# Kernel optimization log

Hardware: AMD Instinct MI355X
Metric: run time of the kernel (lower is better)

The kernel has to match this reference:

```python
import jax, jax.numpy as jnp
import numpy as np

NTYPES = 2
MAXNEI = 128      # maxNeighborNum
M2 = 16
NPER = 256        # atoms per type
B = 4
EMB = [25, 50, 100]
FIT_IN = M2 * EMB[-1]  # 1600
FH = 240


def setup_inputs() -> dict:
    key = jax.random.key(0)
    ks = jax.random.split(key, 16)
    s = 0.1
    inp = {
        "Ri": jax.random.normal(ks[0], (B, NTYPES * NPER, NTYPES * MAXNEI, 4), jnp.float32),
        "emb_W0": jax.random.normal(ks[1], (4, 1, EMB[0]), jnp.float32) * s,
        "emb_b0": jax.random.normal(ks[2], (4, EMB[0]), jnp.float32) * s,
        "emb_W1": jax.random.normal(ks[3], (4, EMB[0], EMB[1]), jnp.float32) * s,
        "emb_b1": jax.random.normal(ks[4], (4, EMB[1]), jnp.float32) * s,
        "emb_W2": jax.random.normal(ks[5], (4, EMB[1], EMB[2]), jnp.float32) * s,
        "emb_b2": jax.random.normal(ks[6], (4, EMB[2]), jnp.float32) * s,
        "fit_W0": jax.random.normal(ks[7], (2, FIT_IN, FH), jnp.float32) * 0.02,
        "fit_b0": jax.random.normal(ks[8], (2, FH), jnp.float32) * s,
        "fit_W1": jax.random.normal(ks[9], (2, FH, FH), jnp.float32) * 0.05,
        "fit_b1": jax.random.normal(ks[10], (2, FH), jnp.float32) * s,
        "fit_W2": jax.random.normal(ks[11], (2, FH, FH), jnp.float32) * 0.05,
        "fit_b2": jax.random.normal(ks[12], (2, FH), jnp.float32) * s,
        "fit_W3": jax.random.normal(ks[13], (2, FH, 1), jnp.float32) * 0.05,
        "fit_b3": jax.random.normal(ks[14], (2, 1), jnp.float32),
    }
    return inp


def _emb(s, W0, b0, W1, b1, W2, b2):
    # DeepMD-style embedding MLP with doubling resnet skips (1->25->50->100)
    h0 = jnp.tanh(s @ W0 + b0)
    h1 = jnp.tanh(h0 @ W1 + b1) + jnp.concatenate([h0, h0], axis=-1)
    h2 = jnp.tanh(h1 @ W2 + b2) + jnp.concatenate([h1, h1], axis=-1)
    return h2


def _fit(d, W0, b0, W1, b1, W2, b2, W3, b3):
    h = jnp.tanh(d @ W0 + b0)
    h = jnp.tanh(h @ W1 + b1) + h   # resnet skip (equal dims)
    h = jnp.tanh(h @ W2 + b2) + h
    return h @ W3 + b3              # [B, N, 1]


def reference(Ri, emb_W0, emb_b0, emb_W1, emb_b1, emb_W2, emb_b2,
              fit_W0, fit_b0, fit_W1, fit_b1, fit_W2, fit_b2, fit_W3, fit_b3):
    type_nums = NTYPES
    Ei_blocks = []
    for i in range(NTYPES):                      # center-atom type
        Ri_i = Ri[:, i * NPER:(i + 1) * NPER]    # [B, NPER, NTYPES*M, 4]
        xyz = None
        for j in range(NTYPES):                  # neighbor type
            blk = Ri_i[:, :, j * MAXNEI:(j + 1) * MAXNEI, :]  # [B,N,M,4]
            S = blk[..., 0:1]                                  # [B,N,M,1]
            e = i * NTYPES + j
            G = _emb(S, emb_W0[e], emb_b0[e], emb_W1[e], emb_b1[e],
                     emb_W2[e], emb_b2[e])                     # [B,N,M,100]
            tmp = jnp.einsum('bnmc,bnmg->bncg', blk, G)        # [B,N,4,100]
            xyz = tmp if xyz is None else xyz + tmp
        xyz = xyz / (MAXNEI * type_nums)
        xyz_b = xyz[..., :M2]                                  # [B,N,4,16]
        DR = jnp.einsum('bncg,bnch->bngh', xyz, xyz_b)         # [B,N,100,16]
        DR = DR.reshape(B, NPER, FIT_IN)
        Ei_i = _fit(DR, fit_W0[i], fit_b0[i], fit_W1[i], fit_b1[i],
                    fit_W2[i], fit_b2[i], fit_W3[i], fit_b3[i])  # [B,N,1]
        Ei_blocks.append(Ei_i)
    Ei = jnp.concatenate(Ei_blocks, axis=1)     # [B, natoms_sum, 1]
    return Ei[..., 0]                            # per-atom energies [B, natoms_sum]
```

## Files before the change

kernel.cpp:

```cpp
#include <hip/hip_runtime.h>
#include <hip/hip_bf16.h>

#define FH 240
#define FIT_IN 1600
#define NK 2048
#define TLO -16.0f
#define TINVH 64.0f

typedef _Float16 h8 __attribute__((ext_vector_type(8)));
typedef float f4v __attribute__((ext_vector_type(4)));

__device__ __forceinline__ float fast_tanh(float x) {
    float e2 = __builtin_amdgcn_exp2f(x * 2.8853900817779268f);
    return 1.0f - 2.0f * __builtin_amdgcn_rcpf(e2 + 1.0f);
}

#define FMA_ROW(r, s) \
    acc[r][0] += (s) * b0.x; acc[r][1] += (s) * b0.y; \
    acc[r][2] += (s) * b0.z; acc[r][3] += (s) * b0.w; \
    acc[r][4] += (s) * b1.x; acc[r][5] += (s) * b1.y; \
    acc[r][6] += (s) * b1.z; acc[r][7] += (s) * b1.w;

#define TOFF_W0   0
#define TOFF_B0   28
#define TOFF_B1   56
#define TOFF_B2   108
#define TOFF_W1   208
#define TOFF_W2   1508
#define TOFF_H0T  6708
#define TOFF_H1T  10008
#define TSMEM     16608

__global__ __launch_bounds__(256) void k_prep(
    const float* __restrict__ eW0, const float* __restrict__ eB0,
    const float* __restrict__ eW1, const float* __restrict__ eB1,
    const float* __restrict__ eW2, const float* __restrict__ eB2,
    float* __restrict__ T,
    const float* __restrict__ fW0, const float* __restrict__ fW1,
    const float* __restrict__ fW2,
    _Float16* __restrict__ W0T, _Float16* __restrict__ W1T,
    _Float16* __restrict__ W2T)
{
    __shared__ float sm[TSMEM];
    const int t = threadIdx.x;

    if (blockIdx.x >= 64) {
        const int bid0 = blockIdx.x - 64;
        const int total = 768000 + 115200 + 115200;
        for (int idx = bid0 * 256 + t; idx < total; idx += 448 * 256) {
            if (idx < 768000) {
                const int tp = idx / 384000, r = idx - tp * 384000;
                const int n = r / 1600, k = r - n * 1600;
                W0T[idx] = (_Float16)fW0[tp * 384000 + k * 240 + n];
            } else if (idx < 883200) {
                const int j = idx - 768000;
                const int tp = j / 57600, r = j - tp * 57600;
                const int n = r / 240, k = r - n * 240;
                W1T[j] = (_Float16)fW1[tp * 57600 + k * 240 + n];
            } else {
                const int j = idx - 883200;
                const int tp = j / 57600, r = j - tp * 57600;
                const int n = r / 240, k = r - n * 240;
                W2T[j] = (_Float16)fW2[tp * 57600 + k * 240 + n];
            }
        }
        return;
    }

    const int w    = t >> 6;
    const int lane = t & 63;
    const int mi   = lane & 7;
    const int gi   = lane >> 3;
    const int mrow = w * 32 + mi * 4;

    const int e  = blockIdx.x >> 4;
    const int k0 = (blockIdx.x & 15) * 128;

    for (int idx = t; idx < 1250; idx += 256) {
        int k = idx / 50, g = idx - k * 50;
        sm[TOFF_W1 + k * 52 + g] = eW1[e * 1250 + idx];
    }
    for (int idx = t; idx < 5000; idx += 256) {
        int k = idx / 100, r = idx - k * 100;
        int half = r / 50, g = r - half * 50;
        sm[TOFF_W2 + k * 104 + half * 52 + g] = eW2[e * 5000 + idx];
    }
    if (t < 25)       { sm[TOFF_W0 + t] = eW0[e * 25 + t]; sm[TOFF_B0 + t] = eB0[e * 25 + t]; }
    else if (t < 75)  { sm[TOFF_B1 + (t - 25)] = eB1[e * 50 + (t - 25)]; }
    else if (t < 175) { sm[TOFF_B2 + (t - 75)] = eB2[e * 100 + (t - 75)]; }
    __syncthreads();

    if (t < 128) {
        const float S = TLO + (float)(k0 + t) * (1.0f / TINVH);
        #pragma unroll
        for (int k = 0; k < 25; ++k)
            sm[TOFF_H0T + k * 132 + t] = fast_tanh(S * sm[TOFF_W0 + k] + sm[TOFF_B0 + k]);
    }
    __syncthreads();

    {
        float acc[4][8];
        #pragma unroll
        for (int r = 0; r < 4; ++r)
            #pragma unroll
            for (int c = 0; c < 8; ++c) acc[r][c] = 0.f;

        #pragma unroll 5
        for (int k = 0; k < 25; ++k) {
            const float4 av = *(const float4*)&sm[TOFF_H0T + k * 132 + mrow];
            const float4 b0 = *(const float4*)&sm[TOFF_W1 + k * 52 + gi * 8];
            const float4 b1 = *(const float4*)&sm[TOFF_W1 + k * 52 + gi * 8 + 4];
            FMA_ROW(0, av.x) FMA_ROW(1, av.y) FMA_ROW(2, av.z) FMA_ROW(3, av.w)
        }
        #pragma unroll
        for (int c = 0; c < 8; ++c) {
            const int g = gi * 8 + c;
            if (g < 50) {
                const int gm = (g < 25) ? g : g - 25;
                const float4 h0r = *(const float4*)&sm[TOFF_H0T + gm * 132 + mrow];
                const float bias = sm[TOFF_B1 + g];
                float4 o;
                o.x = fast_tanh(acc[0][c] + bias) + h0r.x;
                o.y = fast_tanh(acc[1][c] + bias) + h0r.y;
                o.z = fast_tanh(acc[2][c] + bias) + h0r.z;
                o.w = fast_tanh(acc[3][c] + bias) + h0r.w;
                *(float4*)&sm[TOFF_H1T + g * 132 + mrow] = o;
            }
        }
    }
    __syncthreads();

    for (int half = 0; half < 2; ++half) {
        float acc[4][8];
        #pragma unroll
        for (int r = 0; r < 4; ++r)
            #pragma unroll
            for (int c = 0; c < 8; ++c) acc[r][c] = 0.f;

        #pragma unroll 5
        for (int k = 0; k < 50; ++k) {
            const float4 av = *(const float4*)&sm[TOFF_H1T + k * 132 + mrow];
            const float4 b0 = *(const float4*)&sm[TOFF_W2 + k * 104 + half * 52 + gi * 8];
            const float4 b1 = *(const float4*)&sm[TOFF_W2 + k * 104 + half * 52 + gi * 8 + 4];
            FMA_ROW(0, av.x) FMA_ROW(1, av.y) FMA_ROW(2, av.z) FMA_ROW(3, av.w)
        }
        #pragma unroll
        for (int c = 0; c < 8; ++c) {
            const int g = gi * 8 + c;
            if (g < 50) {
                const float4 h1r = *(const float4*)&sm[TOFF_H1T + g * 132 + mrow];
                const float bias = sm[TOFF_B2 + half * 50 + g];
                float* out = T + ((size_t)e * NK + k0 + mrow) * 100 + half * 50 + g;
                out[0]   = fast_tanh(acc[0][c] + bias) + h1r.x;
                out[100] = fast_tanh(acc[1][c] + bias) + h1r.y;
                out[200] = fast_tanh(acc[2][c] + bias) + h1r.z;
                out[300] = fast_tanh(acc[3][c] + bias) + h1r.w;
            }
        }
    }
}

__global__ __launch_bounds__(256) void k_xyz(
    const float* __restrict__ Ri, const float* __restrict__ T,
    _Float16* __restrict__ DRh)
{
    __shared__ float4 sR[256];
    __shared__ float  sF[256];
    __shared__ int    sI[256];
    __shared__ float  sXYZ[400];

    const int t   = threadIdx.x;
    const int blk = blockIdx.x;
    const int b   = blk >> 9;
    const int i   = (blk >> 8) & 1;
    const int n   = blk & 255;

    for (int idx = t; idx < 400; idx += 256) sXYZ[idx] = 0.f;

    {
        const int jj = t >> 7, m = t & 127;
        const size_t row = ((size_t)(b * 512 + i * 256 + n)) * 256 + jj * 128 + m;
        const float4 r = *(const float4*)(Ri + row * 4);
        sR[t] = r;
        float u = (r.x - TLO) * TINVH;
        int ii = (int)u;
        ii = (ii < 0) ? 0 : ((ii > NK - 2) ? NK - 2 : ii);
        sI[t] = ii;
        sF[t] = u - (float)ii;
    }
    __syncthreads();

    const int jj = t >> 7;
    const int g  = t & 127;
    if (g < 100) {
        const float* Te = T + ((size_t)(i * 2 + jj)) * NK * 100 + g;
        float a0 = 0.f, a1 = 0.f, a2 = 0.f, a3 = 0.f;
        #pragma unroll 4
        for (int m = 0; m < 128; ++m) {
            const int s = jj * 128 + m;
            const float4 R = sR[s];
            const float  f = sF[s];
            const float* p = Te + (size_t)sI[s] * 100;
            const float v0 = p[0], v1 = p[100];
            const float G = v0 + f * (v1 - v0);
            a0 += R.x * G; a1 += R.y * G; a2 += R.z * G; a3 += R.w * G;
        }
        atomicAdd(&sXYZ[g],       a0);
        atomicAdd(&sXYZ[100 + g], a1);
        atomicAdd(&sXYZ[200 + g], a2);
        atomicAdd(&sXYZ[300 + g], a3);
    }
    __syncthreads();

    const float inv = 1.0f / 65536.0f;
    _Float16* dr = DRh + (((size_t)i * 4 + b) * 256 + n) * FIT_IN;
    for (int q = t; q < 400; q += 256) {
        const int gg = q >> 2, h0 = (q & 3) * 4;
        ushort4 pk;
        _Float16* ph = (_Float16*)&pk;
        #pragma unroll
        for (int r = 0; r < 4; ++r) {
            const int h = h0 + r;
            const float v = (sXYZ[gg] * sXYZ[h] + sXYZ[100 + gg] * sXYZ[100 + h]
                           + sXYZ[200 + gg] * sXYZ[200 + h] + sXYZ[300 + gg] * sXYZ[300 + h]) * inv;
            ph[r] = (_Float16)v;
        }
        *(ushort4*)(dr + gg * 16 + h0) = pk;
    }
}

__global__ __launch_bounds__(512) void k_fit(
    const _Float16* __restrict__ DRh,
    const _Float16* __restrict__ W0T, const _Float16* __restrict__ W1T,
    const _Float16* __restrict__ W2T,
    const float* __restrict__ fb0, const float* __restrict__ fb1,
    const float* __restrict__ fb2, const float* __restrict__ fW3,
    const float* __restrict__ fb3, float* __restrict__ out)
{
    __shared__ _Float16 sA[16 * 264];
    __shared__ float    hRes[2][8 * 240];

    const int t    = threadIdx.x;
    const int w    = t >> 6;
    const int lane = t & 63;
    const int ln   = lane & 15;
    const int quad = lane >> 4;
    const int r0   = blockIdx.x * 8;
    const int tp   = r0 >> 10;
    const int nf0  = w * 2;
    const int nfr  = (w < 7) ? 2 : 1;

    for (int q = t; q < 16 * 264; q += 512) sA[q] = (_Float16)0.f;

    f4v acc[2];
    acc[0] = (f4v)0.f; acc[1] = (f4v)0.f;
    {
        const _Float16* Arow = DRh + (size_t)(r0 + (ln & 7)) * FIT_IN;
        const _Float16* W0b  = W0T + (size_t)tp * 240 * FIT_IN;
        const _Float16* Bp0  = W0b + (size_t)(nf0 * 16 + ln) * FIT_IN;
        const _Float16* Bp1  = W0b + (size_t)(((nfr > 1) ? nf0 + 1 : nf0) * 16 + ln) * FIT_IN;
        const int kq = quad * 8;

        h8 a_c  = *(const h8*)(Arow + kq);
        h8 b0_c = *(const h8*)(Bp0 + kq);
        h8 b1_c = *(const h8*)(Bp1 + kq);
        h8 a_n  = *(const h8*)(Arow + 32 + kq);
        h8 b0_n = *(const h8*)(Bp0 + 32 + kq);
        h8 b1_n = *(const h8*)(Bp1 + 32 + kq);

        #pragma unroll 2
        for (int s = 0; s < 50; ++s) {
            h8 a_f, b0_f, b1_f;
            if (s + 2 < 50) {
                const int k2 = (s + 2) * 32 + kq;
                a_f  = *(const h8*)(Arow + k2);
                b0_f = *(const h8*)(Bp0 + k2);
                b1_f = *(const h8*)(Bp1 + k2);
            }
            acc[0] = __builtin_amdgcn_mfma_f32_16x16x32_f16(a_c, b0_c, acc[0], 0, 0, 0);
            acc[1] = __builtin_amdgcn_mfma_f32_16x16x32_f16(a_c, b1_c, acc[1], 0, 0, 0);
            a_c = a_n;  b0_c = b0_n;  b1_c = b1_n;
            a_n = a_f;  b0_n = b0_f;  b1_n = b1_f;
        }
    }
    {
        const float* B0 = fb0 + tp * FH;
        #pragma unroll
        for (int nf = 0; nf < 2; ++nf) {
            if (nf < nfr && quad < 2) {
                const int col = (nf0 + nf) * 16 + ln;
                const float bias = B0[col];
                #pragma unroll
                for (int r = 0; r < 4; ++r) {
                    const int m = quad * 4 + r;
                    const float v = fast_tanh(acc[nf][r] + bias);
                    hRes[0][m * 240 + col] = v;
                    sA[m * 264 + col] = (_Float16)v;
                }
            }
        }
    }
    __syncthreads();

    for (int layer = 0; layer < 2; ++layer) {
        const _Float16* Wt = (layer == 0 ? W1T : W2T) + (size_t)tp * FH * FH;
        const float* Bias  = (layer == 0 ? fb1 : fb2) + tp * FH;
        const float* res   = hRes[layer];
        float* outb        = hRes[layer ^ 1];

        const _Float16* Bq0 = Wt + (size_t)(nf0 * 16 + ln) * FH;
        const _Float16* Bq1 = Wt + (size_t)(((nfr > 1) ? nf0 + 1 : nf0) * 16 + ln) * FH;
        const int kq = quad * 8;

        f4v a2[2];
        a2[0] = (f4v)0.f; a2[1] = (f4v)0.f;

        h8 b0_c = *(const h8*)(Bq0 + kq);
        h8 b1_c = *(const h8*)(Bq1 + kq);
        #pragma unroll
        for (int s = 0; s < 8; ++s) {
            h8 b0_n, b1_n;
            if (s + 1 < 8) {
                const int k1 = (s + 1) * 32 + kq;
                b0_n = *(const h8*)(Bq0 + k1);
                b1_n = *(const h8*)(Bq1 + k1);
            }
            const h8 afr = *(const h8*)&sA[ln * 264 + s * 32 + kq];
            a2[0] = __builtin_amdgcn_mfma_f32_16x16x32_f16(afr, b0_c, a2[0], 0, 0, 0);
            a2[1] = __builtin_amdgcn_mfma_f32_16x16x32_f16(afr, b1_c, a2[1], 0, 0, 0);
            b0_c = b0_n;  b1_c = b1_n;
        }
        __syncthreads();
        #pragma unroll
        for (int nf = 0; nf < 2; ++nf) {
            if (nf < nfr && quad < 2) {
                const int col = (nf0 + nf) * 16 + ln;
                const float bias = Bias[col];
                #pragma unroll
                for (int r = 0; r < 4; ++r) {
                    const int m = quad * 4 + r;
                    const float v = fast_tanh(a2[nf][r] + bias) + res[m * 240 + col];
                    outb[m * 240 + col] = v;
                    if (layer == 0) sA[m * 264 + col] = (_Float16)v;
                }
            }
        }
        __syncthreads();
    }

    {
        const float* h2 = hRes[0];
        const float* wv = fW3 + tp * FH;
        const int m = w;
        float s = 0.f;
        #pragma unroll
        for (int k = lane; k < FH; k += 64) s += h2[m * 240 + k] * wv[k];
        #pragma unroll
        for (int off = 32; off > 0; off >>= 1) s += __shfl_down(s, off);
        if (lane == 0) {
            const int gr = r0 + m;
            const int rem = gr & 1023;
            const int b = rem >> 8, n = rem & 255;
            out[b * 512 + tp * 256 + n] = s + fb3[tp];
        }
    }
}

extern "C" void kernel_launch(void* const* d_in, const int* in_sizes, int n_in,
                              void* d_out, int out_size, void* d_ws, size_t ws_size,
                              hipStream_t stream)
{
    const float* Ri  = (const float*)d_in[0];
    const float* eW0 = (const float*)d_in[1];
    const float* eB0 = (const float*)d_in[2];
    const float* eW1 = (const float*)d_in[3];
    const float* eB1 = (const float*)d_in[4];
    const float* eW2 = (const float*)d_in[5];
    const float* eB2 = (const float*)d_in[6];
    const float* fW0 = (const float*)d_in[7];
    const float* fb0 = (const float*)d_in[8];
    const float* fW1 = (const float*)d_in[9];
    const float* fb1 = (const float*)d_in[10];
    const float* fW2 = (const float*)d_in[11];
    const float* fb2 = (const float*)d_in[12];
    const float* fW3 = (const float*)d_in[13];
    const float* fb3 = (const float*)d_in[14];

    char* p = (char*)d_ws;
    float* T   = (float*)p;                 p += (size_t)4 * NK * 100 * 4;
    _Float16* DRh = (_Float16*)p;           p += (size_t)2048 * FIT_IN * 2;
    _Float16* W0T = (_Float16*)p;           p += (size_t)768000 * 2;
    _Float16* W1T = (_Float16*)p;           p += (size_t)115200 * 2;
    _Float16* W2T = (_Float16*)p;           p += (size_t)115200 * 2;

    k_prep<<<dim3(512), dim3(256), 0, stream>>>(eW0, eB0, eW1, eB1, eW2, eB2, T,
                                                fW0, fW1, fW2, W0T, W1T, W2T);
    k_xyz<<<dim3(2048), dim3(256), 0, stream>>>(Ri, T, DRh);
    k_fit<<<dim3(256), dim3(512), 0, stream>>>(DRh, W0T, W1T, W2T,
                                               fb0, fb1, fb2, fW3, fb3,
                                               (float*)d_out);
}
```

Baseline: 172.9 us.

## Split fitting net into tiled MFMA layer-0 kernel and scalar tail kernel

Replaces the single fused fitting kernel with two kernels. The first tiles the 1600x240 first layer over 128-row by 16-column blocks, staging the weight slice in shared memory so it is reused across 128 rows instead of being re-read from global memory by every 8-row block. The second runs the two 240x240 resnet layers and the output dot product with scalar FMAs, two rows per block. This adds an extra launch and an fp32 intermediate buffer written to and read back from global memory, and the tail layers no longer use MFMA.

```diff
diff --git a/kernel.cpp b/kernel.cpp
--- a/kernel.cpp
+++ b/kernel.cpp
@@ -229,138 +229,125 @@
     }
 }
 
-__global__ __launch_bounds__(512) void k_fit(
-    const _Float16* __restrict__ DRh,
-    const _Float16* __restrict__ W0T, const _Float16* __restrict__ W1T,
-    const _Float16* __restrict__ W2T,
-    const float* __restrict__ fb0, const float* __restrict__ fb1,
-    const float* __restrict__ fb2, const float* __restrict__ fW3,
-    const float* __restrict__ fb3, float* __restrict__ out)
-{
-    __shared__ _Float16 sA[16 * 264];
-    __shared__ float    hRes[2][8 * 240];
+__global__ __launch_bounds__(256) void k_fit0(
+    const _Float16* __restrict__ DRh, const _Float16* __restrict__ W0T,
+    const float* __restrict__ fb0, float* __restrict__ hA)
+{
+    __shared__ _Float16 sW[16 * 1608];
 
     const int t    = threadIdx.x;
     const int w    = t >> 6;
     const int lane = t & 63;
     const int ln   = lane & 15;
     const int quad = lane >> 4;
-    const int r0   = blockIdx.x * 8;
-    const int tp   = r0 >> 10;
-    const int nf0  = w * 2;
-    const int nfr  = (w < 7) ? 2 : 1;
-
-    for (int q = t; q < 16 * 264; q += 512) sA[q] = (_Float16)0.f;
-
-    f4v acc[2];
-    acc[0] = (f4v)0.f; acc[1] = (f4v)0.f;
-    {
-        const _Float16* Arow = DRh + (size_t)(r0 + (ln & 7)) * FIT_IN;
-        const _Float16* W0b  = W0T + (size_t)tp * 240 * FIT_IN;
-        const _Float16* Bp0  = W0b + (size_t)(nf0 * 16 + ln) * FIT_IN;
-        const _Float16* Bp1  = W0b + (size_t)(((nfr > 1) ? nf0 + 1 : nf0) * 16 + ln) * FIT_IN;
-        const int kq = quad * 8;
-
-        h8 a_c  = *(const h8*)(Arow + kq);
-        h8 b0_c = *(const h8*)(Bp0 + kq);
-        h8 b1_c = *(const h8*)(Bp1 + kq);
-        h8 a_n  = *(const h8*)(Arow + 32 + kq);
-        h8 b0_n = *(const h8*)(Bp0 + 32 + kq);
-        h8 b1_n = *(const h8*)(Bp1 + 32 + kq);
-
-        #pragma unroll 2
-        for (int s = 0; s < 50; ++s) {
-            h8 a_f, b0_f, b1_f;
-            if (s + 2 < 50) {
-                const int k2 = (s + 2) * 32 + kq;
-                a_f  = *(const h8*)(Arow + k2);
-                b0_f = *(const h8*)(Bp0 + k2);
-                b1_f = *(const h8*)(Bp1 + k2);
-            }
-            acc[0] = __builtin_amdgcn_mfma_f32_16x16x32_f16(a_c, b0_c, acc[0], 0, 0, 0);
-            acc[1] = __builtin_amdgcn_mfma_f32_16x16x32_f16(a_c, b1_c, acc[1], 0, 0, 0);
-            a_c = a_n;  b0_c = b0_n;  b1_c = b1_n;
-            a_n = a_f;  b0_n = b0_f;  b1_n = b1_f;
-        }
-    }
-    {
-        const float* B0 = fb0 + tp * FH;
-        #pragma unroll
-        for (int nf = 0; nf < 2; ++nf) {
-            if (nf < nfr && quad < 2) {
-                const int col = (nf0 + nf) * 16 + ln;
-                const float bias = B0[col];
-                #pragma unroll
-                for (int r = 0; r < 4; ++r) {
-                    const int m = quad * 4 + r;
-                    const float v = fast_tanh(acc[nf][r] + bias);
-                    hRes[0][m * 240 + col] = v;
-                    sA[m * 264 + col] = (_Float16)v;
-                }
-            }
-        }
-    }
+
+    const int m  = blockIdx.x;
+    const int nt = blockIdx.y;
+    const int r0 = m * 128;
+    const int tp = m >> 3;
+    const int n0 = nt * 16;
+
+    const _Float16* Wb = W0T + ((size_t)tp * 240 + n0) * FIT_IN;
+    for (int q = t; q < 6400; q += 256) {
+        const int row = q / 400, kq = (q - row * 400) * 4;
+        *(uint2*)&sW[row * 1608 + kq] = *(const uint2*)(Wb + (size_t)row * FIT_IN + kq);
+    }
+    __syncthreads();
+
+    const int rw = r0 + w * 32;
+    const _Float16* A0 = DRh + (size_t)(rw + ln) * FIT_IN;
+    const _Float16* A1 = A0 + (size_t)16 * FIT_IN;
+    const int kq = quad * 8;
+
+    f4v acc0 = (f4v)0.f, acc1 = (f4v)0.f;
+    h8 a0c = *(const h8*)(A0 + kq);
+    h8 a1c = *(const h8*)(A1 + kq);
+    h8 a0n = *(const h8*)(A0 + 32 + kq);
+    h8 a1n = *(const h8*)(A1 + 32 + kq);
+
+    #pragma unroll 2
+    for (int s = 0; s < 50; ++s) {
+        h8 a0f, a1f;
+        if (s + 2 < 50) {
+            const int k2 = (s + 2) * 32 + kq;
+            a0f = *(const h8*)(A0 + k2);
+            a1f = *(const h8*)(A1 + k2);
+        }
+        const h8 bfr = *(const h8*)&sW[ln * 1608 + s * 32 + kq];
+        acc0 = __builtin_amdgcn_mfma_f32_16x16x32_f16(a0c, bfr, acc0, 0, 0, 0);
+        acc1 = __builtin_amdgcn_mfma_f32_16x16x32_f16(a1c, bfr, acc1, 0, 0, 0);
+        a0c = a0n; a1c = a1n;
+        a0n = a0f; a1n = a1f;
+    }
+
+    const int col  = n0 + ln;
+    const float bias = fb0[tp * FH + col];
+    #pragma unroll
+    for (int r = 0; r < 4; ++r) {
+        const int row0a = rw + quad * 4 + r;
+        const int row1a = rw + 16 + quad * 4 + r;
+        hA[(size_t)row0a * FH + col] = fast_tanh(acc0[r] + bias);
+        hA[(size_t)row1a * FH + col] = fast_tanh(acc1[r] + bias);
+    }
+}
+
+__global__ __launch_bounds__(256) void k_fit_tail(
+    const float* __restrict__ hA,
+    const _Float16* __restrict__ W1T, const _Float16* __restrict__ W2T,
+    const float* __restrict__ fb1, const float* __restrict__ fb2,
+    const float* __restrict__ fW3, const float* __restrict__ fb3,
+    float* __restrict__ out)
+{
+    __shared__ float h[2][2 * FH];
+
+    const int t  = threadIdx.x;
+    const int r0 = blockIdx.x * 2;
+    const int tp = r0 >> 10;
+
+    for (int e = t; e < 2 * FH; e += 256)
+        h[0][e] = hA[(size_t)r0 * FH + e];
     __syncthreads();
 
     for (int layer = 0; layer < 2; ++layer) {
         const _Float16* Wt = (layer == 0 ? W1T : W2T) + (size_t)tp * FH * FH;
-        const float* Bias  = (layer == 0 ? fb1 : fb2) + tp * FH;
-        const float* res   = hRes[layer];
-        float* outb        = hRes[layer ^ 1];
-
-        const _Float16* Bq0 = Wt + (size_t)(nf0 * 16 + ln) * FH;
-        const _Float16* Bq1 = Wt + (size_t)(((nfr > 1) ? nf0 + 1 : nf0) * 16 + ln) * FH;
-        const int kq = quad * 8;
-
-        f4v a2[2];
-        a2[0] = (f4v)0.f; a2[1] = (f4v)0.f;
-
-        h8 b0_c = *(const h8*)(Bq0 + kq);
-        h8 b1_c = *(const h8*)(Bq1 + kq);
-        #pragma unroll
-        for (int s = 0; s < 8; ++s) {
-            h8 b0_n, b1_n;
-            if (s + 1 < 8) {
-                const int k1 = (s + 1) * 32 + kq;
-                b0_n = *(const h8*)(Bq0 + k1);
-                b1_n = *(const h8*)(Bq1 + k1);
+        const float* Bs    = (layer == 0 ? fb1 : fb2) + tp * FH;
+        const float* hin   = h[layer];
+        float* hout        = h[layer ^ 1];
+
+        #pragma unroll
+        for (int half = 0; half < 2; ++half) {
+            const int e = t + half * 256;
+            if (e < 2 * FH) {
+                const int m = (e >= FH) ? 1 : 0;
+                const int c = e - m * FH;
+                const float* hr = hin + m * FH;
+                const _Float16* wr = Wt + (size_t)c * FH;
+                float acc = 0.f;
+                #pragma unroll 6
+                for (int k = 0; k < FH; k += 8) {
+                    const h8 wv8 = *(const h8*)(wr + k);
+                    #pragma unroll
+                    for (int j = 0; j < 8; ++j)
+                        acc += hr[k + j] * (float)wv8[j];
+                }
+                hout[e] = fast_tanh(acc + Bs[c]) + hr[c];
             }
-            const h8 afr = *(const h8*)&sA[ln * 264 + s * 32 + kq];
-            a2[0] = __builtin_amdgcn_mfma_f32_16x16x32_f16(afr, b0_c, a2[0], 0, 0, 0);
-            a2[1] = __builtin_amdgcn_mfma_f32_16x16x32_f16(afr, b1_c, a2[1], 0, 0, 0);
-            b0_c = b0_n;  b1_c = b1_n;
         }
         __syncthreads();
-        #pragma unroll
-        for (int nf = 0; nf < 2; ++nf) {
-            if (nf < nfr && quad < 2) {
-                const int col = (nf0 + nf) * 16 + ln;
-                const float bias = Bias[col];
-                #pragma unroll
-                for (int r = 0; r < 4; ++r) {
-                    const int m = quad * 4 + r;
-                    const float v = fast_tanh(a2[nf][r] + bias) + res[m * 240 + col];
-                    outb[m * 240 + col] = v;
-                    if (layer == 0) sA[m * 264 + col] = (_Float16)v;
-                }
-            }
-        }
-        __syncthreads();
-    }
-
-    {
-        const float* h2 = hRes[0];
+    }
+
+    const int w = t >> 6, lane = t & 63;
+    if (w < 2) {
+        const float* h2 = h[0] + w * FH;
         const float* wv = fW3 + tp * FH;
-        const int m = w;
         float s = 0.f;
         #pragma unroll
-        for (int k = lane; k < FH; k += 64) s += h2[m * 240 + k] * wv[k];
+        for (int k = lane; k < FH; k += 64) s += h2[k] * wv[k];
         #pragma unroll
         for (int off = 32; off > 0; off >>= 1) s += __shfl_down(s, off);
         if (lane == 0) {
-            const int gr = r0 + m;
-            const int rem = gr & 1023;
-            const int b = rem >> 8, n = rem & 255;
+            const int gr = r0 + w;
+            const int b = (gr >> 8) & 3, n = gr & 255;
             out[b * 512 + tp * 256 + n] = s + fb3[tp];
         }
     }
@@ -392,11 +379,14 @@
     _Float16* W0T = (_Float16*)p;           p += (size_t)768000 * 2;
     _Float16* W1T = (_Float16*)p;           p += (size_t)115200 * 2;
     _Float16* W2T = (_Float16*)p;           p += (size_t)115200 * 2;
+    float* hA  = (float*)p;                 p += (size_t)2048 * FH * 4;
 
     k_prep<<<dim3(512), dim3(256), 0, stream>>>(eW0, eB0, eW1, eB1, eW2, eB2, T,
                                                 fW0, fW1, fW2, W0T, W1T, W2T);
     k_xyz<<<dim3(2048), dim3(256), 0, stream>>>(Ri, T, DRh);
-    k_fit<<<dim3(256), dim3(512), 0, stream>>>(DRh, W0T, W1T, W2T,
-                                               fb0, fb1, fb2, fW3, fb3,
-                                               (float*)d_out);
-}
+
+    k_fit0<<<dim3(16, 15), dim3(256), 0, stream>>>(DRh, W0T, fb0, hA);
+
+    k_fit_tail<<<dim3(1024), dim3(256), 0, stream>>>(hA, W1T, W2T, fb1, fb2,
+                                                     fW3, fb3, (float*)d_out);
+}
```

New measurement: 223.4 us. +29.2%, slower.
